# Optimization experiments

Measured on AMD Instinct MI355X. Metric: run time of the kernel, lower is better.

## Reference

```python
import jax, jax.numpy as jnp
from jax import lax
import numpy as np

P = 16      # n_latent
T = 16      # n_frames
ALPHA = 0.5


def conv2d(x, w, b):
    # Conv2d(k=3, stride=2, pad=1), NCHW/OIHW
    y = lax.conv_general_dilated(x, w, (2, 2), ((1, 1), (1, 1)),
                                 dimension_numbers=('NCHW', 'OIHW', 'NCHW'))
    return y + b[None, :, None, None]


def convT2d(x, w, b):
    # ConvTranspose2d(k=3, stride=2, pad=1, output_pad=1): lhs_dilation=2,
    # pad low = k-1-p = 1, pad high = k-1-p+op = 2, kernel flipped, I/O swapped.
    wk = jnp.flip(w, (2, 3)).transpose(1, 0, 2, 3)
    y = lax.conv_general_dilated(x, wk, (1, 1), ((1, 2), (1, 2)),
                                 lhs_dilation=(2, 2),
                                 dimension_numbers=('NCHW', 'OIHW', 'NCHW'))
    return y + b[None, :, None, None]


def build_tridiag(D, Boff, alpha):
    # D: [B, P*P*T], Boff: [B, P*P*(T-1)] -> block-tridiagonal [B, P*T, P*T]
    b = D.shape[0]
    Db = D.reshape(b, T, P, P)
    Bb = Boff.reshape(b, T - 1, P, P)
    blocks = jnp.zeros((b, T, T, P, P), D.dtype)
    i = jnp.arange(T)
    blocks = blocks.at[:, i, i].set(Db)                                # diagonal blocks
    blocks = blocks.at[:, i[1:], i[:-1]].set(Bb)                        # sub-diagonal
    blocks = blocks.at[:, i[:-1], i[1:]].set(Bb.transpose(0, 1, 3, 2))  # super-diagonal (transposed)
    M = blocks.transpose(0, 1, 3, 2, 4).reshape(b, P * T, P * T)
    return M + alpha * jnp.eye(P * T, dtype=D.dtype)


def setup_inputs() -> dict:
    key = jax.random.key(0)
    ks = jax.random.split(key, 20)
    B = 256

    def kaiming(k, shape, fan_in):
        return jax.random.normal(k, shape, jnp.float32) * np.float32(np.sqrt(2.0 / fan_in))

    inp = {}
    inp['x'] = jax.random.normal(ks[0], (B, T, 32, 32), jnp.float32)
    inp['eps'] = jax.random.normal(ks[1], (B, P * T), jnp.float32)
    # encoder convs
    inp['w1'] = kaiming(ks[2], (32, 1, 3, 3), 9);     inp['b1'] = jnp.zeros((32,), jnp.float32)
    inp['w2'] = kaiming(ks[3], (32, 32, 3, 3), 288);  inp['b2'] = jnp.zeros((32,), jnp.float32)
    inp['w3'] = kaiming(ks[4], (64, 32, 3, 3), 288);  inp['b3'] = jnp.zeros((64,), jnp.float32)
    inp['w4'] = kaiming(ks[5], (64, 64, 3, 3), 576);  inp['b4'] = jnp.zeros((64,), jnp.float32)
    inp['w5'] = kaiming(ks[6], (64, 64, 3, 3), 576);  inp['b5'] = jnp.zeros((64,), jnp.float32)
    # encoder fc heads
    F = 64 * T
    inp['fc_mu_w'] = kaiming(ks[7], (P * T, F), F);   inp['fc_mu_b'] = jnp.zeros((P * T,), jnp.float32)
    # tiny std so alpha*I dominates -> precision matrix is PD (valid Cholesky)
    inp['fc_D_w'] = jax.random.normal(ks[8], (P * P * T, F), jnp.float32) * np.float32(3e-5)
    inp['fc_D_b'] = jnp.zeros((P * P * T,), jnp.float32)
    inp['fc_B_w'] = jax.random.normal(ks[9], (P * P * (T - 1), F), jnp.float32) * np.float32(3e-5)
    inp['fc_B_b'] = jnp.zeros((P * P * (T - 1),), jnp.float32)
    # decoder
    inp['fc_dec_w'] = kaiming(ks[10], (F, P * T), P * T); inp['fc_dec_b'] = jnp.zeros((F,), jnp.float32)
    inp['wt5'] = kaiming(ks[11], (64, 64, 3, 3), 576); inp['bt5'] = jnp.zeros((64,), jnp.float32)
    inp['wt4'] = kaiming(ks[12], (64, 64, 3, 3), 576); inp['bt4'] = jnp.zeros((64,), jnp.float32)
    inp['wt3'] = kaiming(ks[13], (64, 32, 3, 3), 576); inp['bt3'] = jnp.zeros((32,), jnp.float32)
    inp['wt2'] = kaiming(ks[14], (32, 32, 3, 3), 288); inp['bt2'] = jnp.zeros((32,), jnp.float32)
    inp['wt1'] = kaiming(ks[15], (32, 1, 3, 3), 288);  inp['bt1'] = jnp.zeros((1,), jnp.float32)
    return inp


def reference(x, eps, w1, b1, w2, b2, w3, b3, w4, b4, w5, b5,
              fc_mu_w, fc_mu_b, fc_D_w, fc_D_b, fc_B_w, fc_B_b,
              fc_dec_w, fc_dec_b, wt5, bt5, wt4, bt4, wt3, bt3,
              wt2, bt2, wt1, bt1):
    Bsz = x.shape[0]
    # ---- encode ----
    h = x.reshape(-1, 1, 32, 32)
    for w, b in ((w1, b1), (w2, b2), (w3, b3), (w4, b4), (w5, b5)):
        h = jax.nn.relu(conv2d(h, w, b))      # ends at [B*T, 64, 1, 1]
    h = h.reshape(Bsz, 64 * T)
    mu = h @ fc_mu_w.T + fc_mu_b              # [B, P*T]
    Dv = h @ fc_D_w.T + fc_D_b                # [B, P*P*T]
    Bv = h @ fc_B_w.T + fc_B_b                # [B, P*P*(T-1)]
    # ---- reparametrize ----
    Pm = build_tridiag(Dv, Bv, ALPHA)         # [B, P*T, P*T]
    L = jnp.linalg.cholesky(Pm)               # lower, uses lower triangle (as torch.cholesky)
    cov = jnp.linalg.inv(L)                   # per-sample inverse of Cholesky factor
    z = mu + jnp.einsum('bij,bj->bi', cov, eps)
    # ---- decode ----
    hd = (z @ fc_dec_w.T + fc_dec_b).reshape(-1, 64, 1, 1)
    for w, b in ((wt5, bt5), (wt4, bt4), (wt3, bt3), (wt2, bt2)):
        hd = jax.nn.elu(convT2d(hd, w, b))
    xr = jax.nn.sigmoid(convT2d(hd, wt1, bt1))  # [B*T, 1, 32, 32]
    return (xr, mu, cov, Pm)
```

## Files before the change

kernel.cpp:

```cpp
#include <hip/hip_runtime.h>
#include <cmath>

#define ALPHA 0.5f

__global__ __launch_bounds__(256) void transpose_all8(
    const float* __restrict__ dw5, const float* __restrict__ dw4,
    const float* __restrict__ dw3, const float* __restrict__ dw2,
    const float* __restrict__ ew2, const float* __restrict__ ew3,
    const float* __restrict__ ew4, const float* __restrict__ ew5,
    float* __restrict__ t5, float* __restrict__ t4,
    float* __restrict__ t3, float* __restrict__ t2,
    float* __restrict__ e2, float* __restrict__ e3,
    float* __restrict__ e4, float* __restrict__ e5)
{
    int idx = blockIdx.x * 256 + threadIdx.x;
    if (idx >= 202752) return;
    const float* w; float* t; int CIN, COUT, loc; bool enc = false;
    if (idx < 36864)       { w = dw5; t = t5; CIN = 64; COUT = 64; loc = idx; }
    else if (idx < 73728)  { w = dw4; t = t4; CIN = 64; COUT = 64; loc = idx - 36864; }
    else if (idx < 92160)  { w = dw3; t = t3; CIN = 64; COUT = 32; loc = idx - 73728; }
    else if (idx < 101376) { w = dw2; t = t2; CIN = 32; COUT = 32; loc = idx - 92160; }
    else if (idx < 110592) { w = ew2; t = e2; CIN = 32; COUT = 32; loc = idx - 101376; enc = true; }
    else if (idx < 129024) { w = ew3; t = e3; CIN = 32; COUT = 64; loc = idx - 110592; enc = true; }
    else if (idx < 165888) { w = ew4; t = e4; CIN = 64; COUT = 64; loc = idx - 129024; enc = true; }
    else                   { w = ew5; t = e5; CIN = 64; COUT = 64; loc = idx - 165888; enc = true; }
    int wk = loc % 9; int r = loc / 9; int ci, co;
    if (enc) { ci = r % CIN;  co = r / CIN;  }
    else     { co = r % COUT; ci = r / COUT; }
    t[wk * CIN * COUT + ci * COUT + co] = w[loc];
}

__device__ __forceinline__ int a1map(int iy, int col) {
    return (col & 7)
         | ((iy & 2) << 2)
         | (((iy ^ (iy >> 2)) & 1) << 4)
         | ((col & 8) << 2)
         | ((iy & 4) << 4)
         | ((iy & 8) << 4);
}

template<int OY, int OX>
__device__ __forceinline__ float c4_cls(
    const float* __restrict__ a3s, const float* __restrict__ w4t,
    float acc, int co)
{
    for (int ci = 0; ci < 64; ci++) {
        #pragma unroll
        for (int ky = 0; ky < 3; ky++) {
            const int iy = 2 * OY - 1 + ky;
            if (iy < 0) continue;
            #pragma unroll
            for (int kx = 0; kx < 3; kx++) {
                const int ix = 2 * OX - 1 + kx;
                if (ix < 0) continue;
                acc = fmaf(a3s[ci * 16 + iy * 4 + ix],
                           w4t[(ky * 3 + kx) * 4096 + ci * 64 + co], acc);
            }
        }
    }
    return acc;
}

__global__ __launch_bounds__(256, 4) void enc_fused(
    const float* __restrict__ x,
    const float* __restrict__ w1,  const float* __restrict__ b1,
    const float* __restrict__ w2t, const float* __restrict__ b2,
    const float* __restrict__ w3t, const float* __restrict__ b3,
    const float* __restrict__ w4t, const float* __restrict__ b4,
    const float* __restrict__ w5t, const float* __restrict__ b5,
    float* __restrict__ hout)
{
    __shared__ __align__(16) float smem[10240];
    float* a1s  = smem;
    float* bse  = smem + 8192;
    float* imgs = bse;
    float* a2s  = bse;
    float* a3s  = smem;
    float* a4s  = smem + 1024;
    float* reds = smem + 1280;

    const int n = blockIdx.x;
    const int tid = threadIdx.x;

    const float* xi = x + n * 1024;
    #pragma unroll
    for (int i = 0; i < 4; i++) {
        int idx = tid + 256 * i;
        int iy = idx >> 5, ix = idx & 31;
        int col = (ix & 1) ? 20 + (ix >> 1) : (ix >> 1);
        imgs[iy * 40 + col] = xi[idx];
    }
    __syncthreads();

    {
        const int oy = tid >> 4, ox = tid & 15;
        float patch[9];
        #pragma unroll
        for (int ky = 0; ky < 3; ky++) {
            const int iy = 2 * oy - 1 + ky;
            #pragma unroll
            for (int kx = 0; kx < 3; kx++) {
                const int ix = 2 * ox - 1 + kx;
                bool v = (iy >= 0) && (ix >= 0);
                int col = (ix & 1) ? 20 + (ix >> 1) : (ix >> 1);
                patch[ky * 3 + kx] = v ? imgs[iy * 40 + col] : 0.f;
            }
        }
        const int ocol = (ox & 1) ? 8 + (ox >> 1) : (ox >> 1);
        const int sidx = a1map(oy, ocol);
        for (int c = 0; c < 32; c++) {
            float acc = b1[c];
            #pragma unroll
            for (int k = 0; k < 9; k++) acc = fmaf(patch[k], w1[c * 9 + k], acc);
            a1s[c * 256 + sidx] = fmaxf(acc, 0.f);
        }
    }
    __syncthreads();

    {
        const int p = tid & 63, oy = p >> 3, ox = p & 7;
        const int c0u = __builtin_amdgcn_readfirstlane(tid >> 6);
        const int cobase = c0u * 8;
        float acc[8];
        #pragma unroll
        for (int r = 0; r < 8; r++) acc[r] = b2[cobase + r];
        int offs[9]; bool val[9];
        #pragma unroll
        for (int ky = 0; ky < 3; ky++) {
            const int iy = 2 * oy - 1 + ky;
            #pragma unroll
            for (int kx = 0; kx < 3; kx++) {
                const int ix = 2 * ox - 1 + kx;
                const bool v = (iy >= 0) && (ix >= 0);
                const int col = (ix & 1) ? 8 + (ix >> 1) : (ix >> 1);
                offs[ky * 3 + kx] = v ? a1map(iy, col) : 0;
                val[ky * 3 + kx] = v;
            }
        }
        for (int ci = 0; ci < 32; ci++) {
            float patch[9];
            #pragma unroll
            for (int k = 0; k < 9; k++)
                patch[k] = val[k] ? a1s[ci * 256 + offs[k]] : 0.f;
            const float* wci = w2t + ci * 32 + cobase;
            #pragma unroll
            for (int k = 0; k < 9; k++) {
                #pragma unroll
                for (int r = 0; r < 8; r++)
                    acc[r] = fmaf(patch[k], wci[k * 1024 + r], acc[r]);
            }
        }
        __syncthreads();
        #pragma unroll
        for (int r = 0; r < 8; r++)
            a2s[(cobase + r) * 64 + p] = fmaxf(acc[r], 0.f);
    }
    __syncthreads();

    {
        const int px = tid & 15, oy = px >> 2, ox = px & 3;
        const int cg = tid >> 4;
        float4 bv = ((const float4*)b3)[cg];
        float acc[4] = {bv.x, bv.y, bv.z, bv.w};
        for (int ci = 0; ci < 32; ci++) {
            float patch[9];
            #pragma unroll
            for (int ky = 0; ky < 3; ky++) {
                const int iy = 2 * oy - 1 + ky;
                #pragma unroll
                for (int kx = 0; kx < 3; kx++) {
                    const int ix = 2 * ox - 1 + kx;
                    bool v = (iy >= 0) && (ix >= 0);
                    patch[ky * 3 + kx] = v ? a2s[ci * 64 + iy * 8 + ix] : 0.f;
                }
            }
            #pragma unroll
            for (int k = 0; k < 9; k++) {
                float4 wv = *(const float4*)(w3t + k * 2048 + ci * 64 + cg * 4);
                acc[0] = fmaf(patch[k], wv.x, acc[0]);
                acc[1] = fmaf(patch[k], wv.y, acc[1]);
                acc[2] = fmaf(patch[k], wv.z, acc[2]);
                acc[3] = fmaf(patch[k], wv.w, acc[3]);
            }
        }
        #pragma unroll
        for (int r = 0; r < 4; r++)
            a3s[(cg * 4 + r) * 16 + px] = fmaxf(acc[r], 0.f);
    }
    __syncthreads();

    {
        const int co = tid & 63;
        const int cls = __builtin_amdgcn_readfirstlane(tid >> 6);
        float acc = b4[co];
        if (cls == 0)      acc = c4_cls<0, 0>(a3s, w4t, acc, co);
        else if (cls == 1) acc = c4_cls<0, 1>(a3s, w4t, acc, co);
        else if (cls == 2) acc = c4_cls<1, 0>(a3s, w4t, acc, co);
        else               acc = c4_cls<1, 1>(a3s, w4t, acc, co);
        a4s[co * 4 + cls] = fmaxf(acc, 0.f);
    }
    __syncthreads();

    {
        const int c = tid & 63, part = tid >> 6;
        float s = 0.f;
        for (int ci = part * 16; ci < part * 16 + 16; ci++) {
            const float* av = a4s + ci * 4;
            s = fmaf(av[0], w5t[4 * 4096 + ci * 64 + c], s);
            s = fmaf(av[1], w5t[5 * 4096 + ci * 64 + c], s);
            s = fmaf(av[2], w5t[7 * 4096 + ci * 64 + c], s);
            s = fmaf(av[3], w5t[8 * 4096 + ci * 64 + c], s);
        }
        reds[part * 64 + c] = s;
    }
    __syncthreads();
    if (tid < 64) {
        float v = b5[tid] + reds[tid] + reds[64 + tid] + reds[128 + tid] + reds[192 + tid];
        hout[n * 64 + tid] = fmaxf(v, 0.f);
    }
}

__global__ __launch_bounds__(256) void pm_zero(float4* __restrict__ Pm4)
{
    Pm4[blockIdx.x * 256 + threadIdx.x] = make_float4(0.f, 0.f, 0.f, 0.f);
}

__global__ __launch_bounds__(256) void fc_enc(
    const float* __restrict__ h,
    const float* __restrict__ wmu, const float* __restrict__ bmu,
    const float* __restrict__ wD,  const float* __restrict__ bD,
    const float* __restrict__ wB,  const float* __restrict__ bB,
    float* __restrict__ mu, float* __restrict__ Pm)
{
    __shared__ float As[32][65];
    __shared__ float Bs[32][65];
    const int tid = threadIdx.x;
    const int m0 = blockIdx.y * 64;
    const int n0 = blockIdx.x * 64;

    const float* wbase; const float* bias; int nloc; int region;
    if (n0 < 256)       { wbase = wmu; bias = bmu; nloc = n0;        region = 0; }
    else if (n0 < 4352) { wbase = wD;  bias = bD;  nloc = n0 - 256;  region = 1; }
    else                { wbase = wB;  bias = bB;  nloc = n0 - 4352; region = 2; }

    const int tx = tid & 15, ty = tid >> 4;
    float acc[4][4] = {};
    for (int k0 = 0; k0 < 1024; k0 += 32) {
        #pragma unroll
        for (int s = 0; s < 8; s++) {
            int l = tid + 256 * s;
            int row = l >> 5, kk = l & 31;
            As[kk][row] = h[(m0 + row) * 1024 + k0 + kk];
            Bs[kk][row] = wbase[(nloc + row) * 1024 + k0 + kk];
        }
        __syncthreads();
        #pragma unroll
        for (int kk = 0; kk < 32; kk++) {
            float av[4], bv[4];
            #pragma unroll
            for (int i = 0; i < 4; i++) av[i] = As[kk][ty * 4 + i];
            #pragma unroll
            for (int j = 0; j < 4; j++) bv[j] = Bs[kk][tx * 4 + j];
            #pragma unroll
            for (int i = 0; i < 4; i++)
                #pragma unroll
                for (int j = 0; j < 4; j++) acc[i][j] = fmaf(av[i], bv[j], acc[i][j]);
        }
        __syncthreads();
    }
    #pragma unroll
    for (int i = 0; i < 4; i++) {
        int m = m0 + ty * 4 + i;
        size_t pbase = (size_t)m * 65536;
        #pragma unroll
        for (int j = 0; j < 4; j++) {
            int nc = nloc + tx * 4 + j;
            float v = acc[i][j] + bias[nc];
            if (region == 0) {
                mu[m * 256 + nc] = v;
            } else {
                int t = nc >> 8, pi = (nc >> 4) & 15, pj = nc & 15;
                if (region == 1) {
                    int row = t * 16 + pi, col = t * 16 + pj;
                    Pm[pbase + row * 256 + col] = v + (pi == pj ? ALPHA : 0.f);
                } else {
                    int row = (t + 1) * 16 + pi, col = t * 16 + pj;
                    Pm[pbase + row * 256 + col] = v;
                    Pm[pbase + col * 256 + row] = v;
                }
            }
        }
    }
}

__global__ __launch_bounds__(64) void chol_band(
    const float* __restrict__ Pm, float* __restrict__ Lb_g)
{
    __shared__ float Lb[256 * 32 + 32];
    __shared__ float Ds[4096];
    __shared__ float Bs2[3840];
    const int b = blockIdx.x, lane = threadIdx.x;
    const float* Pb = Pm + (size_t)b * 65536;
    for (int i = lane; i < 8224; i += 64) Lb[i] = 0.f;
    for (int i = lane; i < 4096; i += 64) {
        int t = i >> 8, r = (i >> 4) & 15, c = i & 15;
        Ds[i] = Pb[(t * 16 + r) * 256 + t * 16 + c];
    }
    for (int i = lane; i < 3840; i += 64) {
        int t = i >> 8, r = (i >> 4) & 15, c = i & 15;
        Bs2[i] = Pb[((t + 1) * 16 + r) * 256 + t * 16 + c];
    }
    __syncthreads();

    const int d = lane;
    for (int j = 0; j < 256; j++) {
        const int i = j + d;
        float s = 0.f;
        if (d < 32 && i < 256) {
            int bi = i >> 4, bj = j >> 4, pi = i & 15, pj = j & 15;
            float a;
            if (bi == bj)           a = Ds[bi * 256 + pi * 16 + pj];
            else if (bi == bj + 1)  a = Bs2[bj * 256 + pi * 16 + pj];
            else                    a = 0.f;

            float c[32], p[32];
            const float* cp = Lb + j * 32;
            #pragma unroll
            for (int q = 0; q < 8; q++)
                *(float4*)(c + 4 * q) = *(const float4*)(cp + 4 * q);
            const float* pp = Lb + i * 32 + d;
            #pragma unroll
            for (int m = 1; m < 32; m++) p[m] = pp[m];

            float s0 = 0.f, s1 = 0.f, s2 = 0.f, s3 = 0.f;
            #pragma unroll
            for (int m = 1; m <= 28; m += 4) {
                s0 = fmaf(p[m],     c[m],     s0);
                s1 = fmaf(p[m + 1], c[m + 1], s1);
                s2 = fmaf(p[m + 2], c[m + 2], s2);
                s3 = fmaf(p[m + 3], c[m + 3], s3);
            }
            s0 = fmaf(p[29], c[29], s0);
            s1 = fmaf(p[30], c[30], s1);
            s2 = fmaf(p[31], c[31], s2);
            s = a - ((s0 + s1) + (s2 + s3));
        }
        float diag = __shfl(s, 0);
        float Ljj = sqrtf(diag);
        if (d == 0)                  Lb[j * 32] = Ljj;
        else if (d < 32 && i < 256)  Lb[i * 32 + d] = s / Ljj;
        __syncthreads();
    }
    for (int i = lane; i < 8192; i += 64) Lb_g[b * 8192 + i] = Lb[i];
}

__global__ __launch_bounds__(256) void inv_band(
    const float* __restrict__ Lb_g, float* __restrict__ cov)
{
    __shared__ __align__(16) float Ls[8192];
    __shared__ float rs[256];
    const int b = blockIdx.x, j = threadIdx.x;
    float* covb = cov + (size_t)b * 65536;

    {
        const float4* src = (const float4*)(Lb_g + b * 8192);
        float4* dst = (float4*)Ls;
        #pragma unroll
        for (int q = 0; q < 8; q++) dst[j + 256 * q] = src[j + 256 * q];
    }
    __syncthreads();
    rs[j] = 1.f / Ls[j * 32];
    __syncthreads();

    const int w = __builtin_amdgcn_readfirstlane(j >> 6);
    const int istart = w * 64;

    for (int i = 0; i < istart; i++) covb[i * 256 + j] = 0.f;

    float g[32];
    #pragma unroll
    for (int q = 0; q < 32; q++) g[q] = 0.f;

    for (int c = istart; c < 256; c += 32) {
        #pragma unroll
        for (int u = 0; u < 32; u++) {
            const int i = c + u;
            const float* Lr = Ls + i * 32;
            float s0 = 0.f, s1 = 0.f, s2 = 0.f, s3 = 0.f;
            #pragma unroll
            for (int d = 1; d < 32; d += 4) {
                s0 = fmaf(Lr[d],     g[(u - d) & 31],     s0);
                if (d + 1 < 32) s1 = fmaf(Lr[d + 1], g[(u - d - 1) & 31], s1);
                if (d + 2 < 32) s2 = fmaf(Lr[d + 2], g[(u - d - 2) & 31], s2);
                if (d + 3 < 32) s3 = fmaf(Lr[d + 3], g[(u - d - 3) & 31], s3);
            }
            float s = (s0 + s1) + (s2 + s3);
            float gi = (((i == j) ? 1.f : 0.f) - s) * rs[i];
            g[u & 31] = gi;
            covb[i * 256 + j] = gi;
        }
    }
}

__global__ __launch_bounds__(256) void zvec_k(
    const float* __restrict__ cov, const float* __restrict__ mu,
    const float* __restrict__ eps, float* __restrict__ z)
{
    __shared__ float es[256];
    const int b = blockIdx.x, i = threadIdx.x;
    es[i] = eps[b * 256 + i];
    __syncthreads();
    const float4* row = (const float4*)(cov + (size_t)b * 65536 + i * 256);
    float s = 0.f;
    #pragma unroll 8
    for (int k = 0; k < 64; k++) {
        float4 v = row[k];
        s = fmaf(v.x, es[4 * k], s);
        s = fmaf(v.y, es[4 * k + 1], s);
        s = fmaf(v.z, es[4 * k + 2], s);
        s = fmaf(v.w, es[4 * k + 3], s);
    }
    z[b * 256 + i] = mu[b * 256 + i] + s;
}

__global__ __launch_bounds__(256) void fc_dec_k(
    const float* __restrict__ z, const float* __restrict__ w,
    const float* __restrict__ bias, float* __restrict__ hd0)
{
    __shared__ float zs[256];
    const int blk = blockIdx.x;
    const int b = blk >> 2;
    const int f = ((blk & 3) << 8) + threadIdx.x;
    zs[threadIdx.x] = z[b * 256 + threadIdx.x];
    __syncthreads();
    const float4* wr = (const float4*)(w + f * 256);
    float s = 0.f;
    #pragma unroll 8
    for (int k = 0; k < 64; k++) {
        float4 v = wr[k];
        s = fmaf(v.x, zs[4 * k], s);
        s = fmaf(v.y, zs[4 * k + 1], s);
        s = fmaf(v.z, zs[4 * k + 2], s);
        s = fmaf(v.w, zs[4 * k + 3], s);
    }
    hd0[b * 1024 + f] = s + bias[f];
}

__global__ __launch_bounds__(256) void mu_fix(
    const float* __restrict__ h, const float* __restrict__ w,
    const float* __restrict__ bias, float* __restrict__ mu)
{
    __shared__ float hs[1024];
    const int b = blockIdx.x, p = threadIdx.x;
    #pragma unroll
    for (int i = 0; i < 4; i++) hs[p + 256 * i] = h[b * 1024 + p + 256 * i];
    __syncthreads();
    const float4* wr = (const float4*)(w + p * 1024);
    float s = 0.f;
    #pragma unroll 8
    for (int k = 0; k < 256; k++) {
        float4 v = wr[k];
        s = fmaf(v.x, hs[4 * k], s);
        s = fmaf(v.y, hs[4 * k + 1], s);
        s = fmaf(v.z, hs[4 * k + 2], s);
        s = fmaf(v.w, hs[4 * k + 3], s);
    }
    mu[b * 256 + p] = s + bias[p];
}

__device__ __forceinline__ float eluf(float v) { return v > 0.f ? v : expf(v) - 1.f; }

template<int PY, int PX, int HIN, int WIN, class F>
__device__ __forceinline__ void for_taps(int ey, int ex, F&& f) {
    if (PY == 0) {
        if (PX == 0) { f(4, ey, ex, true); }
        else         { f(5, ey, ex, true); f(3, ey, ex + 1, ex + 1 < WIN); }
    } else {
        if (PX == 0) { f(7, ey, ex, true); f(1, ey + 1, ex, ey + 1 < HIN); }
        else {
            f(8, ey, ex, true);
            f(6, ey, ex + 1, ex + 1 < WIN);
            f(2, ey + 1, ex, ey + 1 < HIN);
            f(0, ey + 1, ex + 1, (ey + 1 < HIN) && (ex + 1 < WIN));
        }
    }
}

template<int OY>
__device__ __forceinline__ void t4_row(
    const float* __restrict__ wt4t, const float* __restrict__ bt4,
    const float* __restrict__ d1, float* __restrict__ d2, int co)
{
    float a0 = 0.f, a1 = 0.f, a2 = 0.f, a3 = 0.f;
    const float* wb = wt4t + co;
    for (int ci = 0; ci < 64; ci++) {
        const float* base = d1 + ci * 12;
        if (OY % 2 == 0) {
            float4 r = *(const float4*)(base + (OY / 2) * 4);
            float w10 = wb[3 * 4096 + ci * 64];
            float w11 = wb[4 * 4096 + ci * 64];
            float w12 = wb[5 * 4096 + ci * 64];
            a0 = fmaf(r.x, w11, a0);
            a1 = fmaf(r.x, w12, a1); a1 = fmaf(r.y, w10, a1);
            a2 = fmaf(r.y, w11, a2);
            a3 = fmaf(r.y, w12, a3); a3 = fmaf(r.z, w10, a3);
        } else {
            float4 ra = *(const float4*)(base + ((OY - 1) / 2) * 4);
            float4 rb = *(const float4*)(base + ((OY + 1) / 2) * 4);
            float w20 = wb[6 * 4096 + ci * 64], w21 = wb[7 * 4096 + ci * 64], w22 = wb[8 * 4096 + ci * 64];
            float w00 = wb[0 * 4096 + ci * 64], w01 = wb[1 * 4096 + ci * 64], w02 = wb[2 * 4096 + ci * 64];
            a0 = fmaf(ra.x, w21, a0); a0 = fmaf(rb.x, w01, a0);
            a1 = fmaf(ra.x, w22, a1); a1 = fmaf(ra.y, w20, a1);
            a1 = fmaf(rb.x, w02, a1); a1 = fmaf(rb.y, w00, a1);
            a2 = fmaf(ra.y, w21, a2); a2 = fmaf(rb.y, w01, a2);
            a3 = fmaf(ra.y, w22, a3); a3 = fmaf(ra.z, w20, a3);
            a3 = fmaf(rb.y, w02, a3); a3 = fmaf(rb.z, w00, a3);
        }
    }
    float b = bt4[co];
    float4 o = make_float4(eluf(a0 + b), eluf(a1 + b), eluf(a2 + b), eluf(a3 + b));
    *(float4*)(d2 + co * 44 + OY * 8) = o;
}

template<int M>
__device__ __forceinline__ void xrow(float* acc, const float* R, float w0, float w1, float w2)
{
    #pragma unroll
    for (int m = 0; m < M; m++) {
        acc[2 * m]     = fmaf(R[m], w1, acc[2 * m]);
        acc[2 * m + 1] = fmaf(R[m], w2, acc[2 * m + 1]);
        acc[2 * m + 1] = fmaf(R[m + 1], w0, acc[2 * m + 1]);
    }
}

__global__ __launch_bounds__(256) void dec_fused(
    const float* __restrict__ hd0,
    const float* __restrict__ wt5t, const float* __restrict__ bt5,
    const float* __restrict__ wt4t, const float* __restrict__ bt4,
    const float* __restrict__ wt3t, const float* __restrict__ bt3,
    const float* __restrict__ wt2t, const float* __restrict__ bt2,
    const float* __restrict__ wt1,  const float* __restrict__ bt1,
    float* __restrict__ xr)
{
    __shared__ __align__(16) float smem[11776];
    float* d0  = smem;
    float* d1  = smem + 64;
    float* d2  = smem + 832;
    float* scr = smem + 3648;
    float* d4  = smem;
    float* d3  = smem + 8320;

    const int n = blockIdx.x, tid = threadIdx.x;

    for (int i = tid; i < 3584; i += 256) smem[64 + i] = 0.f;
    for (int i = tid; i < 3456; i += 256) d3[i] = 0.f;
    if (tid < 64) d0[tid] = hd0[n * 64 + tid];
    __syncthreads();

    {
        const int co = tid & 63;
        const int wv = __builtin_amdgcn_readfirstlane(tid >> 6);
        const int oy = wv >> 1, ox = wv & 1;
        const int wk = (oy + 1) * 3 + (ox + 1);
        const float* wp = wt5t + wk * 4096 + co;
        float s = bt5[co];
        for (int ci = 0; ci < 64; ci++)
            s = fmaf(d0[ci], wp[ci * 64], s);
        d1[co * 12 + oy * 4 + ox] = eluf(s);
    }
    __syncthreads();

    {
        const int co = tid & 63;
        const int oyw = __builtin_amdgcn_readfirstlane(tid >> 6);
        if (oyw == 0)      t4_row<0>(wt4t, bt4, d1, d2, co);
        else if (oyw == 1) t4_row<1>(wt4t, bt4, d1, d2, co);
        else if (oyw == 2) t4_row<2>(wt4t, bt4, d1, d2, co);
        else               t4_row<3>(wt4t, bt4, d1, d2, co);
    }
    __syncthreads();

    {
        const int co = tid & 31, pr = (tid >> 5) & 3, cih = tid >> 7;
        const int e = (pr & 1) ? 7 - pr : pr;
        const int o = (pr & 1) ? pr : 7 - pr;
        const int iy_e = e >> 1, iy_o2 = (o - 1) >> 1, iy_o0 = (o + 1) >> 1;
        float acce[8] = {}, acco[8] = {};
        const float* wb = wt3t + co;
        for (int c = 0; c < 32; c++) {
            const int ci = cih * 32 + c;
            const float* base = d2 + ci * 44;
            float re[8], ro2[8], ro0[8];
            *(float4*)(re)      = *(const float4*)(base + iy_e * 8);
            *(float4*)(re + 4)  = *(const float4*)(base + iy_e * 8 + 4);
            *(float4*)(ro2)     = *(const float4*)(base + iy_o2 * 8);
            *(float4*)(ro2 + 4) = *(const float4*)(base + iy_o2 * 8 + 4);
            *(float4*)(ro0)     = *(const float4*)(base + iy_o0 * 8);
            *(float4*)(ro0 + 4) = *(const float4*)(base + iy_o0 * 8 + 4);
            float w10 = wb[3 * 2048 + ci * 32], w11 = wb[4 * 2048 + ci * 32], w12 = wb[5 * 2048 + ci * 32];
            float w20 = wb[6 * 2048 + ci * 32], w21 = wb[7 * 2048 + ci * 32], w22 = wb[8 * 2048 + ci * 32];
            float w00 = wb[0 * 2048 + ci * 32], w01 = wb[1 * 2048 + ci * 32], w02 = wb[2 * 2048 + ci * 32];
            xrow<4>(acce, re, w10, w11, w12);
            xrow<4>(acco, ro2, w20, w21, w22);
            xrow<4>(acco, ro0, w00, w01, w02);
        }
        if (cih == 1) {
            float* s = scr + (tid - 128) * 20;
            #pragma unroll
            for (int k = 0; k < 8; k++) { s[k] = acce[k]; s[8 + k] = acco[k]; }
        }
        __syncthreads();
        if (cih == 0) {
            const float* s = scr + tid * 20;
            const float b = bt3[co];
            float* oe = d3 + co * 108 + e * 12;
            float* oo = d3 + co * 108 + o * 12;
            #pragma unroll
            for (int k = 0; k < 8; k++) {
                oe[k] = eluf(acce[k] + s[k] + b);
                oo[k] = eluf(acco[k] + s[8 + k] + b);
            }
        }
    }
    __syncthreads();

    {
        const int co = tid & 31, org = tid >> 5;
        float acc0[16] = {}, acc1[16] = {};
        const float* wb = wt2t + co;
        for (int ci = 0; ci < 32; ci++) {
            const float* base = d3 + ci * 108 + org * 12;
            float A[12], B[12];
            #pragma unroll
            for (int q = 0; q < 3; q++) {
                *(float4*)(A + 4 * q) = *(const float4*)(base + 4 * q);
                *(float4*)(B + 4 * q) = *(const float4*)(base + 12 + 4 * q);
            }
            float w10 = wb[3 * 1024 + ci * 32], w11 = wb[4 * 1024 + ci * 32], w12 = wb[5 * 1024 + ci * 32];
            float w20 = wb[6 * 1024 + ci * 32], w21 = wb[7 * 1024 + ci * 32], w22 = wb[8 * 1024 + ci * 32];
            float w00 = wb[0 * 1024 + ci * 32], w01 = wb[1 * 1024 + ci * 32], w02 = wb[2 * 1024 + ci * 32];
            xrow<8>(acc0, A, w10, w11, w12);
            xrow<8>(acc1, A, w20, w21, w22);
            xrow<8>(acc1, B, w00, w01, w02);
        }
        const float b = bt2[co];
        float* o0 = d4 + co * 260 + (2 * org) * 16;
        float* o1 = o0 + 16;
        #pragma unroll
        for (int q = 0; q < 4; q++) {
            float4 v0 = make_float4(eluf(acc0[4 * q] + b), eluf(acc0[4 * q + 1] + b),
                                    eluf(acc0[4 * q + 2] + b), eluf(acc0[4 * q + 3] + b));
            float4 v1 = make_float4(eluf(acc1[4 * q] + b), eluf(acc1[4 * q + 1] + b),
                                    eluf(acc1[4 * q + 2] + b), eluf(acc1[4 * q + 3] + b));
            *(float4*)(o0 + 4 * q) = v0;
            *(float4*)(o1 + 4 * q) = v1;
        }
    }
    __syncthreads();

    {
        const int ey = tid >> 4, ex = tid & 15;
        const float bb = bt1[0];
        float* xi = xr + n * 1024;
        float acc[4] = {};
        for (int ci = 0; ci < 32; ci++) {
            const float* a = d4 + ci * 260;
            const float* w = wt1 + ci * 9;
            for_taps<0, 0, 16, 16>(ey, ex, [&](int wk, int iy, int ix, bool v) {
                acc[0] = fmaf(v ? a[iy * 16 + ix] : 0.f, w[wk], acc[0]); });
            for_taps<0, 1, 16, 16>(ey, ex, [&](int wk, int iy, int ix, bool v) {
                acc[1] = fmaf(v ? a[iy * 16 + ix] : 0.f, w[wk], acc[1]); });
            for_taps<1, 0, 16, 16>(ey, ex, [&](int wk, int iy, int ix, bool v) {
                acc[2] = fmaf(v ? a[iy * 16 + ix] : 0.f, w[wk], acc[2]); });
            for_taps<1, 1, 16, 16>(ey, ex, [&](int wk, int iy, int ix, bool v) {
                acc[3] = fmaf(v ? a[iy * 16 + ix] : 0.f, w[wk], acc[3]); });
        }
        xi[(2 * ey) * 32 + 2 * ex]         = 1.f / (1.f + expf(-(acc[0] + bb)));
        xi[(2 * ey) * 32 + 2 * ex + 1]     = 1.f / (1.f + expf(-(acc[1] + bb)));
        xi[(2 * ey + 1) * 32 + 2 * ex]     = 1.f / (1.f + expf(-(acc[2] + bb)));
        xi[(2 * ey + 1) * 32 + 2 * ex + 1] = 1.f / (1.f + expf(-(acc[3] + bb)));
    }
}

extern "C" void kernel_launch(void* const* d_in, const int* in_sizes, int n_in,
                              void* d_out, int out_size, void* d_ws, size_t ws_size,
                              hipStream_t stream)
{
    (void)in_sizes; (void)n_in; (void)out_size; (void)ws_size;
    const float* x    = (const float*)d_in[0];
    const float* eps  = (const float*)d_in[1];
    const float* w1 = (const float*)d_in[2];  const float* b1 = (const float*)d_in[3];
    const float* w2 = (const float*)d_in[4];  const float* b2 = (const float*)d_in[5];
    const float* w3 = (const float*)d_in[6];  const float* b3 = (const float*)d_in[7];
    const float* w4 = (const float*)d_in[8];  const float* b4 = (const float*)d_in[9];
    const float* w5 = (const float*)d_in[10]; const float* b5 = (const float*)d_in[11];
    const float* fc_mu_w = (const float*)d_in[12]; const float* fc_mu_b = (const float*)d_in[13];
    const float* fc_D_w  = (const float*)d_in[14]; const float* fc_D_b  = (const float*)d_in[15];
    const float* fc_B_w  = (const float*)d_in[16]; const float* fc_B_b  = (const float*)d_in[17];
    const float* fc_dec_w = (const float*)d_in[18]; const float* fc_dec_b = (const float*)d_in[19];
    const float* wt5 = (const float*)d_in[20]; const float* bt5 = (const float*)d_in[21];
    const float* wt4 = (const float*)d_in[22]; const float* bt4 = (const float*)d_in[23];
    const float* wt3 = (const float*)d_in[24]; const float* bt3 = (const float*)d_in[25];
    const float* wt2 = (const float*)d_in[26]; const float* bt2 = (const float*)d_in[27];
    const float* wt1 = (const float*)d_in[28]; const float* bt1 = (const float*)d_in[29];

    float* ws   = (float*)d_ws;
    float* h    = ws;
    float* Lb   = ws + 262144;
    float* z    = ws + 2359296;
    float* hd0  = ws + 2424832;
    float* wt5t = ws + 2686976;
    float* wt4t = ws + 2723840;
    float* wt3t = ws + 2760704;
    float* wt2t = ws + 2779136;
    float* w2t  = ws + 2788352;
    float* w3t  = ws + 2797568;
    float* w4t  = ws + 2816000;
    float* w5t  = ws + 2852864;

    float* out = (float*)d_out;
    float* xr  = out;
    float* mu  = out + 4194304;
    float* cov = out + 4259840;
    float* Pm  = out + 21037056;

    transpose_all8<<<792, 256, 0, stream>>>(wt5, wt4, wt3, wt2, w2, w3, w4, w5,
                                            wt5t, wt4t, wt3t, wt2t, w2t, w3t, w4t, w5t);
    enc_fused<<<4096, 256, 0, stream>>>(x, w1, b1, w2t, b2, w3t, b3, w4t, b4, w5t, b5, h);
    pm_zero<<<16384, 256, 0, stream>>>((float4*)Pm);
    fc_enc<<<dim3(128, 4), 256, 0, stream>>>(h, fc_mu_w, fc_mu_b, fc_D_w, fc_D_b,
                                             fc_B_w, fc_B_b, mu, Pm);
    chol_band<<<256, 64, 0, stream>>>(Pm, Lb);
    inv_band<<<256, 256, 0, stream>>>(Lb, cov);
    zvec_k<<<256, 256, 0, stream>>>(cov, mu, eps, z);
    fc_dec_k<<<1024, 256, 0, stream>>>(z, fc_dec_w, fc_dec_b, hd0);
    dec_fused<<<4096, 256, 0, stream>>>(hd0, wt5t, bt5, wt4t, bt4, wt3t, bt3,
                                        wt2t, bt2, wt1, bt1, xr);
    mu_fix<<<256, 256, 0, stream>>>(h, fc_mu_w, fc_mu_b, mu);
}
```

Before: 1.030 ms.

## Split conv4 over input channels so each weight load feeds all four outputs

```diff
diff --git a/kernel.cpp b/kernel.cpp
--- a/kernel.cpp
+++ b/kernel.cpp
@@ -39,28 +39,6 @@
          | ((iy & 8) << 4);
 }
 
-template<int OY, int OX>
-__device__ __forceinline__ float c4_cls(
-    const float* __restrict__ a3s, const float* __restrict__ w4t,
-    float acc, int co)
-{
-    for (int ci = 0; ci < 64; ci++) {
-        #pragma unroll
-        for (int ky = 0; ky < 3; ky++) {
-            const int iy = 2 * OY - 1 + ky;
-            if (iy < 0) continue;
-            #pragma unroll
-            for (int kx = 0; kx < 3; kx++) {
-                const int ix = 2 * OX - 1 + kx;
-                if (ix < 0) continue;
-                acc = fmaf(a3s[ci * 16 + iy * 4 + ix],
-                           w4t[(ky * 3 + kx) * 4096 + ci * 64 + co], acc);
-            }
-        }
-    }
-    return acc;
-}
-
 __global__ __launch_bounds__(256, 4) void enc_fused(
     const float* __restrict__ x,
     const float* __restrict__ w1,  const float* __restrict__ b1,
@@ -191,13 +169,48 @@
 
     {
         const int co = tid & 63;
-        const int cls = __builtin_amdgcn_readfirstlane(tid >> 6);
-        float acc = b4[co];
-        if (cls == 0)      acc = c4_cls<0, 0>(a3s, w4t, acc, co);
-        else if (cls == 1) acc = c4_cls<0, 1>(a3s, w4t, acc, co);
-        else if (cls == 2) acc = c4_cls<1, 0>(a3s, w4t, acc, co);
-        else               acc = c4_cls<1, 1>(a3s, w4t, acc, co);
-        a4s[co * 4 + cls] = fmaxf(acc, 0.f);
+        const int part = __builtin_amdgcn_readfirstlane(tid >> 6);
+        float a0 = 0.f, a1 = 0.f, a2 = 0.f, a3 = 0.f;
+        for (int ci = part * 16; ci < part * 16 + 16; ci++) {
+            const float* wp = w4t + ci * 64 + co;
+            const float w0 = wp[0];
+            const float w1 = wp[4096];
+            const float w2 = wp[8192];
+            const float w3 = wp[12288];
+            const float w4 = wp[16384];
+            const float w5 = wp[20480];
+            const float w6 = wp[24576];
+            const float w7 = wp[28672];
+            const float w8 = wp[32768];
+            const float4 r0 = *(const float4*)(a3s + ci * 16);
+            const float4 r1 = *(const float4*)(a3s + ci * 16 + 4);
+            const float4 r2 = *(const float4*)(a3s + ci * 16 + 8);
+            const float4 r3 = *(const float4*)(a3s + ci * 16 + 12);
+            a0 = fmaf(r0.x, w4, a0); a0 = fmaf(r0.y, w5, a0);
+            a0 = fmaf(r1.x, w7, a0); a0 = fmaf(r1.y, w8, a0);
+            a1 = fmaf(r0.y, w3, a1); a1 = fmaf(r0.z, w4, a1); a1 = fmaf(r0.w, w5, a1);
+            a1 = fmaf(r1.y, w6, a1); a1 = fmaf(r1.z, w7, a1); a1 = fmaf(r1.w, w8, a1);
+            a2 = fmaf(r1.x, w1, a2); a2 = fmaf(r1.y, w2, a2);
+            a2 = fmaf(r2.x, w4, a2); a2 = fmaf(r2.y, w5, a2);
+            a2 = fmaf(r3.x, w7, a2); a2 = fmaf(r3.y, w8, a2);
+            a3 = fmaf(r1.y, w0, a3); a3 = fmaf(r1.z, w1, a3); a3 = fmaf(r1.w, w2, a3);
+            a3 = fmaf(r2.y, w3, a3); a3 = fmaf(r2.z, w4, a3); a3 = fmaf(r2.w, w5, a3);
+            a3 = fmaf(r3.y, w6, a3); a3 = fmaf(r3.z, w7, a3); a3 = fmaf(r3.w, w8, a3);
+        }
+        float* reds2 = bse;
+        reds2[part * 256 +   0 + co] = a0;
+        reds2[part * 256 +  64 + co] = a1;
+        reds2[part * 256 + 128 + co] = a2;
+        reds2[part * 256 + 192 + co] = a3;
+        __syncthreads();
+        {
+            const int co2 = tid & 63;
+            const int cls2 = __builtin_amdgcn_readfirstlane(tid >> 6);
+            float s = b4[co2]
+                    + reds2[      cls2 * 64 + co2] + reds2[256 + cls2 * 64 + co2]
+                    + reds2[512 + cls2 * 64 + co2] + reds2[768 + cls2 * 64 + co2];
+            a4s[co2 * 4 + cls2] = fmaxf(s, 0.f);
+        }
     }
     __syncthreads();
 
@@ -205,11 +218,11 @@
         const int c = tid & 63, part = tid >> 6;
         float s = 0.f;
         for (int ci = part * 16; ci < part * 16 + 16; ci++) {
-            const float* av = a4s + ci * 4;
-            s = fmaf(av[0], w5t[4 * 4096 + ci * 64 + c], s);
-            s = fmaf(av[1], w5t[5 * 4096 + ci * 64 + c], s);
-            s = fmaf(av[2], w5t[7 * 4096 + ci * 64 + c], s);
-            s = fmaf(av[3], w5t[8 * 4096 + ci * 64 + c], s);
+            const float4 av = *(const float4*)(a4s + ci * 4);
+            s = fmaf(av.x, w5t[4 * 4096 + ci * 64 + c], s);
+            s = fmaf(av.y, w5t[5 * 4096 + ci * 64 + c], s);
+            s = fmaf(av.z, w5t[7 * 4096 + ci * 64 + c], s);
+            s = fmaf(av.w, w5t[8 * 4096 + ci * 64 + c], s);
         }
         reds[part * 64 + c] = s;
     }
```

Result: faster. 995.5 us (-3.4%).
